# Performance work log

Measured on AMD Instinct MI355X. Metric: run time of the kernel, lower is better.

Reference implementation:

```python
import jax, jax.numpy as jnp
import numpy as np

B = 512      # batch per stream
L = 600      # audio length (22 chunks of 75, step 25)
DIM = 256    # model dim
H = 8        # num heads (each head is full-width, per original code)
CH = [1, DIM // 4, DIM // 2, DIM]
KS = [26, 26, 25]
EPS = 1e-5
N_CHUNKS, CHUNK, STEP = 22, 75, 25


def setup_inputs() -> dict:
    key = jax.random.key(0)
    ks = iter(jax.random.split(key, 40))
    def rn(shape, scale=0.05):
        return jax.random.normal(next(ks), shape, jnp.float32) * scale
    inp = {}
    inp["audio_vec1"] = jax.random.normal(next(ks), (B, 1, L), jnp.float32)
    inp["audio_vec2"] = jax.random.normal(next(ks), (B, 1, L), jnp.float32)
    for i in range(3):
        inp[f"conv_w{i+1}"] = rn((CH[i + 1], CH[i], KS[i]))  # OIH, torch Conv1d layout
        inp[f"conv_b{i+1}"] = rn((CH[i + 1],))
        inp[f"bn_g{i+1}"] = jnp.ones((CH[i + 1],), jnp.float32)
        inp[f"bn_b{i+1}"] = jnp.zeros((CH[i + 1],), jnp.float32)
        inp[f"bn_m{i+1}"] = rn((CH[i + 1],))
        inp[f"bn_v{i+1}"] = jnp.ones((CH[i + 1],), jnp.float32)
    # per-head Q/K/V projections (stored [H, in, out]; torch Linear is x @ W.T + b)
    inp["Wq"] = rn((H, DIM, DIM)); inp["bq"] = rn((H, DIM))
    inp["Wk"] = rn((H, DIM, DIM)); inp["bk"] = rn((H, DIM))
    inp["Wv"] = rn((H, DIM, DIM)); inp["bv"] = rn((H, DIM))
    inp["fca_w"] = rn((H * DIM, DIM)); inp["fca_b"] = rn((DIM,))
    inp["fc_w"] = rn((DIM, DIM)); inp["fc_b"] = rn((DIM,))
    return inp


def _chunks(x):
    # x: [B, 1, L] -> [B*22, 1, 75] (batched chunks, chunk-major within each example)
    idx = jnp.arange(N_CHUNKS)[:, None] * STEP + jnp.arange(CHUNK)[None, :]  # [22, 75]
    c = x[:, :, idx]                      # [B, 1, 22, 75]
    return c.transpose(0, 2, 1, 3).reshape(-1, 1, CHUNK)


def _block(x, w, b, g, bt, m, v):
    # Conv1d (valid) + BatchNorm (eval) + Swish; dropout is identity in eval.
    y = jax.lax.conv_general_dilated(
        x, w, window_strides=(1,), padding="VALID",
        dimension_numbers=("NCH", "OIH", "NCH")) + b[None, :, None]
    scale = g * jax.lax.rsqrt(v + EPS)
    y = (y - m[None, :, None]) * scale[None, :, None] + bt[None, :, None]
    return y * jax.nn.sigmoid(y)


def _forward(audio_vec1, audio_vec2,
             conv_w1, conv_b1, bn_g1, bn_b1, bn_m1, bn_v1,
             conv_w2, conv_b2, bn_g2, bn_b2, bn_m2, bn_v2,
             conv_w3, conv_b3, bn_g3, bn_b3, bn_m3, bn_v3,
             Wq, bq, Wk, bk, Wv, bv, fca_w, fca_b, fc_w, fc_b):
    # Batch both streams and all 22 chunks through one conv stack.
    X = jnp.concatenate([_chunks(audio_vec1), _chunks(audio_vec2)], axis=0)  # [2*B*22,1,75]
    X = _block(X, conv_w1, conv_b1, bn_g1, bn_b1, bn_m1, bn_v1)  # [., 64, 50]
    X = _block(X, conv_w2, conv_b2, bn_g2, bn_b2, bn_m2, bn_v2)  # [., 128, 25]
    X = _block(X, conv_w3, conv_b3, bn_g3, bn_b3, bn_m3, bn_v3)  # [., 256, 1]
    feat = X[:, :, 0].reshape(-1, N_CHUNKS, DIM)  # [2B, 22, 256]

    # Multi-head attention: 8 independent full-width heads, no 1/sqrt(d) scaling.
    Q = jnp.einsum("bse,heo->bhso", feat, Wq) + bq[None, :, None, :]
    K = jnp.einsum("bse,heo->bhso", feat, Wk) + bk[None, :, None, :]
    V = jnp.einsum("bse,heo->bhso", feat, Wv) + bv[None, :, None, :]
    A = jax.nn.softmax(jnp.einsum("bhso,bhto->bhst", Q, K), axis=-1)
    O = jnp.einsum("bhst,bhto->bhso", A, V)          # [2B, H, 22, 256]
    O = O.transpose(0, 2, 1, 3).reshape(O.shape[0], N_CHUNKS, H * DIM)
    out = O @ fca_w + fca_b                            # [2B, 22, 256]

    pooled = out.mean(axis=1)                          # [2B, 256]
    y = pooled @ fc_w + fc_b                           # [2B, 256]
    nb = audio_vec1.shape[0]
    return y[:nb], y[nb:]


def reference(audio_vec1, audio_vec2,
              conv_w1, conv_b1, bn_g1, bn_b1, bn_m1, bn_v1,
              conv_w2, conv_b2, bn_g2, bn_b2, bn_m2, bn_v2,
              conv_w3, conv_b3, bn_g3, bn_b3, bn_m3, bn_v3,
              Wq, bq, Wk, bk, Wv, bv, fca_w, fca_b, fc_w, fc_b):
    return _forward(audio_vec1, audio_vec2,
                    conv_w1, conv_b1, bn_g1, bn_b1, bn_m1, bn_v1,
                    conv_w2, conv_b2, bn_g2, bn_b2, bn_m2, bn_v2,
                    conv_w3, conv_b3, bn_g3, bn_b3, bn_m3, bn_v3,
                    Wq, bq, Wk, bk, Wv, bv, fca_w, fca_b, fc_w, fc_b)
```

## Files before the change

kernel.cpp:

```cpp
#include <hip/hip_runtime.h>
#include <hip/hip_bf16.h>
#include <math.h>

#define NSEQ 22528
#define HALFSEQ 11264

typedef __attribute__((ext_vector_type(8))) short short8;
typedef __attribute__((ext_vector_type(4))) float f32x4;
typedef __attribute__((ext_vector_type(4))) ushort ushort4v;

__device__ __forceinline__ ushort f2bf(float x) {
    __hip_bfloat16 h = __float2bfloat16(x);
    return *reinterpret_cast<ushort*>(&h);
}
__device__ __forceinline__ float bf2f(ushort u) {
    unsigned v = ((unsigned)u) << 16;
    return *reinterpret_cast<float*>(&v);
}

__global__ void k_transpose(const float* __restrict__ in, float* __restrict__ out,
                            int Bn, int R, int C) {
    int idx = blockIdx.x * 256 + threadIdx.x;
    int total = Bn * R * C;
    if (idx >= total) return;
    int b = idx / (R * C);
    int rem = idx - b * R * C;
    int c = rem / R;
    int r = rem - c * R;
    out[idx] = in[(b * R + r) * C + c];
}

__global__ void k_prep_w2(const float* __restrict__ w2, ushort* __restrict__ w2f) {
    int idx = blockIdx.x * 256 + threadIdx.x;
    if (idx >= 212992) return;
    int j = idx & 7;
    int lane = (idx >> 3) & 63;
    int mt = (idx >> 9) & 7;
    int kt = idx >> 12;
    int oc = mt * 16 + (lane & 15);
    int k = kt * 32 + ((lane >> 4) << 3) + j;
    int t = k >> 6;
    int ic = k & 63;
    w2f[idx] = f2bf(w2[(oc * 64 + ic) * 26 + t]);
}
__global__ void k_prep_w3(const float* __restrict__ w3, ushort* __restrict__ w3f) {
    int idx = blockIdx.x * 256 + threadIdx.x;
    if (idx >= 819200) return;
    int j = idx & 7;
    int lane = (idx >> 3) & 63;
    int mt = (idx >> 9) & 15;
    int kt = idx >> 13;
    int oc = mt * 16 + (lane & 15);
    int k = kt * 32 + ((lane >> 4) << 3) + j;
    int ic = k & 127;
    int pos = k >> 7;
    w3f[idx] = f2bf(w3[oc * 3200 + ic * 25 + pos]);
}

__global__ __launch_bounds__(256) void k_prep_attn_m(
    const float* __restrict__ Wq, const float* __restrict__ WkT,
    float* __restrict__ M)
{
    const int h = blockIdx.x >> 4;
    const int e0 = (blockIdx.x & 15) * 16;
    const int tid = threadIdx.x;
    __shared__ float sq[16][256];
    for (int idx = tid; idx < 4096; idx += 256) {
        int r = idx >> 8;
        int c = idx & 255;
        sq[r][c] = Wq[(size_t)(h * 256 + e0 + r) * 256 + c];
    }
    __syncthreads();
    float acc[16];
    #pragma unroll
    for (int r = 0; r < 16; ++r) acc[r] = 0.f;
    const float* wkt = WkT + (size_t)h * 65536 + tid;
    for (int o = 0; o < 256; ++o) {
        float wk = wkt[o * 256];
        #pragma unroll
        for (int r = 0; r < 16; ++r) acc[r] += sq[r][o] * wk;
    }
    #pragma unroll
    for (int r = 0; r < 16; ++r)
        M[(size_t)(h * 256 + e0 + r) * 256 + tid] = acc[r];
}

__global__ void k_prep_mfrag(const float* __restrict__ M, ushort* __restrict__ Mfrag) {
    int idx = blockIdx.x * 256 + threadIdx.x;
    int j = idx & 7;
    int lane = (idx >> 3) & 63;
    int mt = (idx >> 9) & 15;
    int kt = (idx >> 13) & 7;
    int h = idx >> 16;
    int e = kt * 32 + ((lane >> 4) << 3) + j;
    int o = mt * 16 + (lane & 15);
    Mfrag[idx] = f2bf(M[(size_t)(h * 256 + e) * 256 + o]);
}

__global__ __launch_bounds__(256) void k_prep_kb(
    const float* __restrict__ Wk, const float* __restrict__ bq,
    float* __restrict__ kb)
{
    const int h = blockIdx.x;
    const int tid = threadIdx.x;
    __shared__ float sbq[256];
    sbq[tid] = bq[h * 256 + tid];
    __syncthreads();
    const float* wk = Wk + (size_t)(h * 256 + tid) * 256;
    float a = 0.f;
    for (int o = 0; o < 256; ++o) a += wk[o] * sbq[o];
    kb[h * 256 + tid] = a;
}

__global__ __launch_bounds__(256) void k_prep_F(
    const float* __restrict__ Wv, const float* __restrict__ fca_w,
    float* __restrict__ F)
{
    const int h = blockIdx.x >> 4;
    const int e0 = (blockIdx.x & 15) * 16;
    const int tid = threadIdx.x;
    __shared__ float sq[16][256];
    for (int idx = tid; idx < 4096; idx += 256) {
        int r = idx >> 8;
        int c = idx & 255;
        sq[r][c] = Wv[(size_t)h * 65536 + (e0 + r) * 256 + c];
    }
    __syncthreads();
    float acc[16];
    #pragma unroll
    for (int r = 0; r < 16; ++r) acc[r] = 0.f;
    for (int o = 0; o < 256; ++o) {
        float w = fca_w[(size_t)(h * 256 + o) * 256 + tid];
        #pragma unroll
        for (int r = 0; r < 16; ++r) acc[r] += sq[r][o] * w;
    }
    #pragma unroll
    for (int r = 0; r < 16; ++r)
        F[(size_t)(h * 256 + e0 + r) * 256 + tid] = acc[r];
}

__global__ __launch_bounds__(256) void k_prep_bvc(
    const float* __restrict__ bv, const float* __restrict__ fca_w,
    const float* __restrict__ fca_b, float* __restrict__ bvc)
{
    const int tid = threadIdx.x;
    __shared__ float sbv[2048];
    for (int i = tid; i < 2048; i += 256) sbv[i] = bv[i];
    __syncthreads();
    float acc = fca_b[tid];
    for (int k = 0; k < 2048; ++k) acc += sbv[k] * fca_w[(size_t)k * 256 + tid];
    bvc[tid] = acc;
}

__global__ __launch_bounds__(256, 4) void k_conv(
    const float* __restrict__ av1, const float* __restrict__ av2,
    const float* __restrict__ w1,
    const float* __restrict__ b1c, const float* __restrict__ g1,
    const float* __restrict__ be1, const float* __restrict__ m1, const float* __restrict__ v1,
    const ushort* __restrict__ w2f,
    const float* __restrict__ b2c, const float* __restrict__ g2,
    const float* __restrict__ be2, const float* __restrict__ m2, const float* __restrict__ v2,
    ushort* __restrict__ a2f, int seqoff)
{
    __shared__ ushort s_a1[4 * 3200];
    __shared__ ushort s_w1f[2048];
    __shared__ ushort s_xb[4][80];
    __shared__ float s_sc1[64], s_sh1[64], s_sc2[128], s_sh2[128];

    const int tid = threadIdx.x;
    const int lane = tid & 63;
    const int wv = tid >> 6;
    const int l15 = lane & 15;
    const int grp = lane >> 4;
    const int lseq0 = blockIdx.x * 4;
    const int gseq0 = seqoff + lseq0;

    for (int s = 0; s < 4; ++s) {
        int seq = gseq0 + s;
        const float* src;
        if (seq < HALFSEQ) { int b = seq / 22; int n = seq - b * 22; src = av1 + b * 600 + n * 25; }
        else { int q = seq - HALFSEQ; int b = q / 22; int n = q - b * 22; src = av2 + b * 600 + n * 25; }
        if (tid < 80) s_xb[s][tid] = f2bf((tid < 75) ? src[tid] : 0.f);
    }
    for (int idx = tid; idx < 2048; idx += 256) {
        int j = idx & 7;
        int ln = (idx >> 3) & 63;
        int mt = idx >> 9;
        int oc = mt * 16 + (ln & 15);
        int k = ((ln >> 4) << 3) + j;
        s_w1f[idx] = (k < 26) ? f2bf(w1[oc * 26 + k]) : (ushort)0;
    }
    if (tid < 64) { float A = g1[tid] * rsqrtf(v1[tid] + 1e-5f); s_sc1[tid] = A; s_sh1[tid] = (b1c[tid] - m1[tid]) * A + be1[tid]; }
    if (tid < 128) { float A = g2[tid] * rsqrtf(v2[tid] + 1e-5f); s_sc2[tid] = A; s_sh2[tid] = (b2c[tid] - m2[tid]) * A + be2[tid]; }
    __syncthreads();

    {
        short8 a1f[4];
        #pragma unroll
        for (int mt = 0; mt < 4; ++mt)
            a1f[mt] = *(const short8*)(s_w1f + mt * 512 + lane * 8);

        for (int nt = wv; nt < 13; nt += 4) {
            int n = nt * 16 + l15;
            int s = (n >= 50) + (n >= 100) + (n >= 150);
            int p = n - s * 50;
            if (p > 49) p = 49;
            short8 bf;
            #pragma unroll
            for (int j = 0; j < 8; ++j) {
                int t = grp * 8 + j;
                bf[j] = (t < 26) ? (short)s_xb[s][p + t] : (short)0;
            }
            f32x4 acc1[4];
            #pragma unroll
            for (int mt = 0; mt < 4; ++mt) {
                acc1[mt] = (f32x4){0.f, 0.f, 0.f, 0.f};
                acc1[mt] = __builtin_amdgcn_mfma_f32_16x16x32_bf16(a1f[mt], bf, acc1[mt], 0, 0, 0);
            }
            if (n < 200) {
                #pragma unroll
                for (int mt = 0; mt < 4; ++mt) {
                    #pragma unroll
                    for (int r = 0; r < 4; ++r) {
                        int oc = mt * 16 + grp * 4 + r;
                        float y = acc1[mt][r] * s_sc1[oc] + s_sh1[oc];
                        y = y / (1.f + __expf(-y));
                        int boff = s * 6400 + p * 128 + ((oc * 2) ^ ((p & 7) << 4));
                        *(ushort*)((char*)s_a1 + boff) = f2bf(y);
                    }
                }
            }
        }
    }
    __syncthreads();

    {
        const int mset = wv >> 1;
        const int nset = wv & 1;
        const int NT = nset ? 3 : 4;

        int nbase[4], nrow[4];
        #pragma unroll
        for (int ni = 0; ni < 4; ++ni) {
            int n = (nset * 4 + ni) * 16 + l15;
            int s = n / 25; if (s > 3) s = 3;
            int p = n - s * 25; if (p > 24) p = 24;
            nbase[ni] = s * 6400;
            nrow[ni] = p;
        }

        f32x4 acc[4][4];
        #pragma unroll
        for (int mi = 0; mi < 4; ++mi)
            #pragma unroll
            for (int ni = 0; ni < 4; ++ni)
                acc[mi][ni] = (f32x4){0.f, 0.f, 0.f, 0.f};

        const ushort* wfp = w2f + (size_t)(mset * 4) * 512 + lane * 8;
        short8 afn[4];
        #pragma unroll
        for (int mi = 0; mi < 4; ++mi) afn[mi] = *(const short8*)(wfp + mi * 512);

        for (int kt = 0; kt < 52; ++kt) {
            const int t = kt >> 1;
            const int ic0b = ((kt & 1) * 32 + grp * 8) * 2;
            short8 af[4];
            #pragma unroll
            for (int mi = 0; mi < 4; ++mi) af[mi] = afn[mi];
            if (kt < 51) {
                #pragma unroll
                for (int mi = 0; mi < 4; ++mi)
                    afn[mi] = *(const short8*)(wfp + (kt + 1) * 4096 + mi * 512);
            }
            #pragma unroll
            for (int ni = 0; ni < 4; ++ni) {
                if (ni >= NT) break;
                int row = nrow[ni] + t;
                int boff = nbase[ni] + row * 128 + (ic0b ^ ((row & 7) << 4));
                short8 bf = *(const short8*)((const char*)s_a1 + boff);
                #pragma unroll
                for (int mi = 0; mi < 4; ++mi)
                    acc[mi][ni] = __builtin_amdgcn_mfma_f32_16x16x32_bf16(af[mi], bf, acc[mi][ni], 0, 0, 0);
            }
        }

        #pragma unroll
        for (int mi = 0; mi < 4; ++mi) {
            const int ocb = mset * 64 + mi * 16 + grp * 4;
            const int grp_dst = (ocb & 31) >> 3;
            const int jb = ocb & 7;
            const int kthi = ocb >> 5;
            #pragma unroll
            for (int ni = 0; ni < 4; ++ni) {
                if (ni >= NT) break;
                int n = (nset * 4 + ni) * 16 + l15;
                if (n < 100) {
                    int s = n / 25;
                    int p = n - s * 25;
                    int seq = lseq0 + s;
                    int kt3 = p * 4 + kthi;
                    ushort4v u;
                    #pragma unroll
                    for (int r = 0; r < 4; ++r) {
                        float y = acc[mi][ni][r] * s_sc2[ocb + r] + s_sh2[ocb + r];
                        y = y / (1.f + __expf(-y));
                        u[r] = f2bf(y);
                    }
                    *(ushort4v*)(a2f + (((size_t)(seq >> 4) * 100 + kt3) << 9)
                                 + ((seq & 15) + 16 * grp_dst) * 8 + jb) = u;
                }
            }
        }
    }
}

__global__ __launch_bounds__(256) void k_conv3(
    const ushort* __restrict__ a2f, const ushort* __restrict__ w3f,
    const float* __restrict__ b3c, const float* __restrict__ g3,
    const float* __restrict__ be3, const float* __restrict__ m3, const float* __restrict__ v3,
    float* __restrict__ feat, int seqoff)
{
    const int tid = threadIdx.x;
    const int lane = tid & 63;
    const int wv = tid >> 6;
    const int l15 = lane & 15;
    const int grp = lane >> 4;
    const int lseq0 = blockIdx.x * 32;

    f32x4 acc3[4][2];
    #pragma unroll
    for (int mi = 0; mi < 4; ++mi)
        #pragma unroll
        for (int nt = 0; nt < 2; ++nt)
            acc3[mi][nt] = (f32x4){0.f, 0.f, 0.f, 0.f};

    const ushort* bp = a2f + ((size_t)(lseq0 >> 4) * 100) * 512 + lane * 8;
    const ushort* ap = w3f + (size_t)(wv * 4) * 512 + lane * 8;

    for (int kt = 0; kt < 100; ++kt) {
        short8 bf0 = *(const short8*)(bp + (size_t)kt * 512);
        short8 bf1 = *(const short8*)(bp + (size_t)(100 + kt) * 512);
        #pragma unroll
        for (int mi = 0; mi < 4; ++mi) {
            short8 af = *(const short8*)(ap + (size_t)kt * 8192 + mi * 512);
            acc3[mi][0] = __builtin_amdgcn_mfma_f32_16x16x32_bf16(af, bf0, acc3[mi][0], 0, 0, 0);
            acc3[mi][1] = __builtin_amdgcn_mfma_f32_16x16x32_bf16(af, bf1, acc3[mi][1], 0, 0, 0);
        }
    }

    #pragma unroll
    for (int nt = 0; nt < 2; ++nt) {
        int gseq = seqoff + lseq0 + nt * 16 + l15;
        #pragma unroll
        for (int mi = 0; mi < 4; ++mi) {
            int oc = wv * 64 + mi * 16 + grp * 4;
            float4 o4;
            #pragma unroll
            for (int r = 0; r < 4; ++r) {
                float A = g3[oc + r] * rsqrtf(v3[oc + r] + 1e-5f);
                float y = acc3[mi][nt][r] * A + (b3c[oc + r] - m3[oc + r]) * A + be3[oc + r];
                ((float*)&o4)[r] = y / (1.f + __expf(-y));
            }
            *(float4*)(feat + (size_t)gseq * 256 + oc) = o4;
        }
    }
}

__global__ __launch_bounds__(256, 2) void k_attn_f(
    const float* __restrict__ feat, const ushort* __restrict__ Mfrag,
    const float* __restrict__ kb, float* __restrict__ fbar_all)
{
    const int g = blockIdx.x;
    const int tid = threadIdx.x;
    const int lane = tid & 63;
    const int wv = tid >> 6;
    const int l15 = lane & 15;
    const int grp = lane >> 4;

    __shared__ __align__(16) float sfL[22 * 260];
    __shared__ __align__(16) ushort sfb[32 * 256];
    __shared__ __align__(16) ushort sG[32 * 256];
    __shared__ float sS[22 * 24];
    __shared__ float sbet[8][24];
    __shared__ float sab[24];

    const float* fsrc = feat + (size_t)g * 5632;
    for (int idx = tid; idx < 8192; idx += 256) {
        int s = idx >> 8;
        int e = idx & 255;
        float f = 0.f;
        if (s < 22) { f = fsrc[s * 256 + e]; sfL[s * 260 + e] = f; }
        int byte = s * 512 + ((e * 2) ^ ((s & 7) << 4));
        *(ushort*)((char*)sfb + byte) = f2bf(f);
    }
    __syncthreads();

    if (tid < 176) {
        int t = tid >> 3;
        int h = tid & 7;
        const float* kr = kb + h * 256;
        const float* fr = sfL + t * 260;
        float a = 0.f;
        for (int e = 0; e < 256; ++e) a += fr[e] * kr[e];
        sbet[h][t] = a;
    }
    __syncthreads();

    for (int h = 0; h < 8; ++h) {
        {
            f32x4 accg[2][4];
            #pragma unroll
            for (int mt = 0; mt < 2; ++mt)
                #pragma unroll
                for (int fi = 0; fi < 4; ++fi)
                    accg[mt][fi] = (f32x4){0.f, 0.f, 0.f, 0.f};

            const ushort* mfb = Mfrag + (size_t)h * 65536;
            for (int kt = 0; kt < 8; ++kt) {
                int e0b = (kt * 32 + grp * 8) * 2;
                int rA0 = l15, rA1 = 16 + l15;
                short8 af0 = *(const short8*)((const char*)sfb + rA0 * 512 + (e0b ^ ((rA0 & 7) << 4)));
                short8 af1 = *(const short8*)((const char*)sfb + rA1 * 512 + (e0b ^ ((rA1 & 7) << 4)));
                #pragma unroll
                for (int fi = 0; fi < 4; ++fi) {
                    int ft = wv * 4 + fi;
                    short8 bfm = *(const short8*)(mfb + (size_t)((kt * 16 + ft) << 9) + lane * 8);
                    accg[0][fi] = __builtin_amdgcn_mfma_f32_16x16x32_bf16(af0, bfm, accg[0][fi], 0, 0, 0);
                    accg[1][fi] = __builtin_amdgcn_mfma_f32_16x16x32_bf16(af1, bfm, accg[1][fi], 0, 0, 0);
                }
            }
            #pragma unroll
            for (int mt = 0; mt < 2; ++mt) {
                #pragma unroll
                for (int fi = 0; fi < 4; ++fi) {
                    int f = (wv * 4 + fi) * 16 + l15;
                    #pragma unroll
                    for (int r = 0; r < 4; ++r) {
                        int s = mt * 16 + grp * 4 + r;
                        if (s < 22) {
                            int byte = s * 512 + ((f * 2) ^ ((s & 7) << 4));
                            *(ushort*)((char*)sG + byte) = f2bf(accg[mt][fi][r]);
                        }
                    }
                }
            }
        }
        __syncthreads();

        {
            int mt2 = wv >> 1;
            int nt2 = wv & 1;
            f32x4 sacc = (f32x4){0.f, 0.f, 0.f, 0.f};
            int sA = mt2 * 16 + l15;
            int tB = nt2 * 16 + l15;
            for (int kt = 0; kt < 8; ++kt) {
                int f0b = (kt * 32 + grp * 8) * 2;
                short8 ga = *(const short8*)((const char*)sG + sA * 512 + (f0b ^ ((sA & 7) << 4)));
                short8 fb = *(const short8*)((const char*)sfb + tB * 512 + (f0b ^ ((tB & 7) << 4)));
                sacc = __builtin_amdgcn_mfma_f32_16x16x32_bf16(ga, fb, sacc, 0, 0, 0);
            }
            #pragma unroll
            for (int r = 0; r < 4; ++r) {
                int s = mt2 * 16 + grp * 4 + r;
                int t = nt2 * 16 + l15;
                if (s < 22 && t < 22) sS[s * 24 + t] = sacc[r] + sbet[h][t];
            }
        }
        __syncthreads();

        if (tid < 22) {
            int s = tid;
            float mx = -1e30f;
            #pragma unroll
            for (int t = 0; t < 22; ++t) mx = fmaxf(mx, sS[s * 24 + t]);
            float ex[22];
            float sum = 0.f;
            #pragma unroll
            for (int t = 0; t < 22; ++t) { float e2 = __expf(sS[s * 24 + t] - mx); ex[t] = e2; sum += e2; }
            float inv = 1.f / sum;
            #pragma unroll
            for (int t = 0; t < 22; ++t) sS[s * 24 + t] = ex[t] * inv;
        }
        __syncthreads();
        if (tid < 22) {
            int t = tid;
            float a = 0.f;
            #pragma unroll
            for (int s = 0; s < 22; ++s) a += sS[s * 24 + t];
            sab[t] = a * (1.f / 22.f);
        }
        __syncthreads();

        {
            float a = 0.f;
            #pragma unroll
            for (int t = 0; t < 22; ++t) a += sab[t] * sfL[t * 260 + tid];
            fbar_all[((size_t)g * 8 + h) * 256 + tid] = a;
        }
    }
}

__global__ __launch_bounds__(256) void k_pool(
    const float* __restrict__ fbar_all, const float* __restrict__ F,
    const float* __restrict__ bvc,
    const float* __restrict__ fc_w, const float* __restrict__ fc_b,
    float* __restrict__ out)
{
    const int g0 = blockIdx.x * 4;
    const int tid = threadIdx.x;
    __shared__ __align__(16) float sfb[32 * 256];
    __shared__ __align__(16) float sp[4 * 256];
    for (int idx = tid; idx < 8192; idx += 256)
        sfb[idx] = fbar_all[(size_t)g0 * 8 * 256 + idx];
    __syncthreads();

    float p[4];
    float bb = bvc[tid];
    #pragma unroll
    for (int j = 0; j < 4; ++j) p[j] = bb;
    for (int k = 0; k < 2048; ++k) {
        float f = F[(size_t)k * 256 + tid];
        #pragma unroll
        for (int j = 0; j < 4; ++j) p[j] += sfb[j * 2048 + k] * f;
    }
    #pragma unroll
    for (int j = 0; j < 4; ++j) sp[j * 256 + tid] = p[j];
    __syncthreads();

    float y[4];
    float fb = fc_b[tid];
    #pragma unroll
    for (int j = 0; j < 4; ++j) y[j] = fb;
    for (int e = 0; e < 256; ++e) {
        float w = fc_w[(size_t)e * 256 + tid];
        #pragma unroll
        for (int j = 0; j < 4; ++j) y[j] += sp[j * 256 + e] * w;
    }
    #pragma unroll
    for (int j = 0; j < 4; ++j)
        out[(size_t)(g0 + j) * 256 + tid] = y[j];
}

extern "C" void kernel_launch(void* const* d_in, const int* in_sizes, int n_in,
                              void* d_out, int out_size, void* d_ws, size_t ws_size,
                              hipStream_t stream) {
    (void)in_sizes; (void)n_in; (void)out_size;

    const float* av1   = (const float*)d_in[0];
    const float* av2   = (const float*)d_in[1];
    const float* w1    = (const float*)d_in[2];
    const float* b1c   = (const float*)d_in[3];
    const float* g1    = (const float*)d_in[4];
    const float* be1   = (const float*)d_in[5];
    const float* m1    = (const float*)d_in[6];
    const float* v1    = (const float*)d_in[7];
    const float* w2    = (const float*)d_in[8];
    const float* b2c   = (const float*)d_in[9];
    const float* g2    = (const float*)d_in[10];
    const float* be2   = (const float*)d_in[11];
    const float* m2    = (const float*)d_in[12];
    const float* v2    = (const float*)d_in[13];
    const float* w3    = (const float*)d_in[14];
    const float* b3c   = (const float*)d_in[15];
    const float* g3    = (const float*)d_in[16];
    const float* be3   = (const float*)d_in[17];
    const float* m3    = (const float*)d_in[18];
    const float* v3    = (const float*)d_in[19];
    const float* Wq    = (const float*)d_in[20];
    const float* bq    = (const float*)d_in[21];
    const float* Wk    = (const float*)d_in[22];
    const float* bk    = (const float*)d_in[23];
    const float* Wv    = (const float*)d_in[24];
    const float* bv    = (const float*)d_in[25];
    const float* fca_w = (const float*)d_in[26];
    const float* fca_b = (const float*)d_in[27];
    const float* fc_w  = (const float*)d_in[28];
    const float* fc_b  = (const float*)d_in[29];
    (void)bk;

    float* ws = (float*)d_ws;
    float* feat = ws;
    float* Mm   = feat + 5767168;
    float* WkT  = Mm + 524288;
    float* kb   = WkT + 524288;
    float* bvc  = kb + 2048;
    float* F    = bvc + 256;
    float* fbar = F + 524288;
    ushort* w2f = (ushort*)(fbar + 2097152);
    ushort* w3f = w2f + 212992;
    ushort* mfr = w3f + 819200;
    ushort* region = mfr + 524288;

    size_t base_bytes = (size_t)((char*)region - (char*)d_ws);
    size_t budget = (ws_size > base_bytes + 4096) ? (ws_size - base_bytes - 4096) : 0;
    int ncA = 16;
    const int cand[5] = {1, 2, 4, 8, 16};
    for (int i = 0; i < 5; ++i) { if ((size_t)144179200 / cand[i] <= budget) { ncA = cand[i]; break; } }
    const int seqsA = NSEQ / ncA;

    k_prep_w2<<<832, 256, 0, stream>>>(w2, w2f);
    k_prep_w3<<<3200, 256, 0, stream>>>(w3, w3f);
    k_transpose<<<2048, 256, 0, stream>>>(Wk, WkT, 8, 256, 256);
    k_prep_attn_m<<<128, 256, 0, stream>>>(Wq, WkT, Mm);
    k_prep_mfrag<<<2048, 256, 0, stream>>>(Mm, mfr);
    k_prep_kb<<<8, 256, 0, stream>>>(Wk, bq, kb);
    k_prep_F<<<128, 256, 0, stream>>>(Wv, fca_w, F);
    k_prep_bvc<<<1, 256, 0, stream>>>(bv, fca_w, fca_b, bvc);

    ushort* a2f = region;
    for (int c = 0; c < ncA; ++c) {
        int seqoff = c * seqsA;
        k_conv<<<seqsA / 4, 256, 0, stream>>>(av1, av2,
            w1, b1c, g1, be1, m1, v1,
            w2f, b2c, g2, be2, m2, v2,
            a2f, seqoff);
        k_conv3<<<seqsA / 32, 256, 0, stream>>>(a2f, w3f,
            b3c, g3, be3, m3, v3, feat, seqoff);
    }

    k_attn_f<<<1024, 256, 0, stream>>>(feat, mfr, kb, fbar);
    k_pool<<<256, 256, 0, stream>>>(fbar, F, bvc, fc_w, fc_b, (float*)d_out);
}
```

Before: 666.3 us.

## Merge prep kernels, widen conv2 block to 8 sequences, enlarge conv3 tile

```diff
diff --git a/kernel.cpp b/kernel.cpp
--- a/kernel.cpp
+++ b/kernel.cpp
@@ -18,43 +18,88 @@
     return *reinterpret_cast<float*>(&v);
 }
 
-__global__ void k_transpose(const float* __restrict__ in, float* __restrict__ out,
-                            int Bn, int R, int C) {
-    int idx = blockIdx.x * 256 + threadIdx.x;
-    int total = Bn * R * C;
-    if (idx >= total) return;
-    int b = idx / (R * C);
-    int rem = idx - b * R * C;
-    int c = rem / R;
-    int r = rem - c * R;
-    out[idx] = in[(b * R + r) * C + c];
-}
-
-__global__ void k_prep_w2(const float* __restrict__ w2, ushort* __restrict__ w2f) {
-    int idx = blockIdx.x * 256 + threadIdx.x;
-    if (idx >= 212992) return;
-    int j = idx & 7;
-    int lane = (idx >> 3) & 63;
-    int mt = (idx >> 9) & 7;
-    int kt = idx >> 12;
-    int oc = mt * 16 + (lane & 15);
-    int k = kt * 32 + ((lane >> 4) << 3) + j;
-    int t = k >> 6;
-    int ic = k & 63;
-    w2f[idx] = f2bf(w2[(oc * 64 + ic) * 26 + t]);
-}
-__global__ void k_prep_w3(const float* __restrict__ w3, ushort* __restrict__ w3f) {
-    int idx = blockIdx.x * 256 + threadIdx.x;
-    if (idx >= 819200) return;
-    int j = idx & 7;
-    int lane = (idx >> 3) & 63;
-    int mt = (idx >> 9) & 15;
-    int kt = idx >> 13;
-    int oc = mt * 16 + (lane & 15);
-    int k = kt * 32 + ((lane >> 4) << 3) + j;
-    int ic = k & 127;
-    int pos = k >> 7;
-    w3f[idx] = f2bf(w3[oc * 3200 + ic * 25 + pos]);
+__global__ __launch_bounds__(256) void k_prep_misc(
+    const float* __restrict__ w2, ushort* __restrict__ w2f,
+    const float* __restrict__ w3, ushort* __restrict__ w3f,
+    const float* __restrict__ Wk, float* __restrict__ WkT,
+    const float* __restrict__ bq, float* __restrict__ kb,
+    const float* __restrict__ bv, const float* __restrict__ fca_w,
+    const float* __restrict__ fca_b, float* __restrict__ bvc,
+    const float* __restrict__ Wv, float* __restrict__ F)
+{
+    __shared__ float smem[16 * 256];
+    const int bid = blockIdx.x;
+    const int tid = threadIdx.x;
+
+    if (bid < 832) {
+        int idx = bid * 256 + tid;
+        if (idx < 212992) {
+            int j = idx & 7;
+            int lane = (idx >> 3) & 63;
+            int mt = (idx >> 9) & 7;
+            int kt = idx >> 12;
+            int oc = mt * 16 + (lane & 15);
+            int k = kt * 32 + ((lane >> 4) << 3) + j;
+            int t = k >> 6;
+            int ic = k & 63;
+            w2f[idx] = f2bf(w2[(oc * 64 + ic) * 26 + t]);
+        }
+    } else if (bid < 4032) {
+        int idx = (bid - 832) * 256 + tid;
+        if (idx < 819200) {
+            int j = idx & 7;
+            int lane = (idx >> 3) & 63;
+            int mt = (idx >> 9) & 15;
+            int kt = idx >> 13;
+            int oc = mt * 16 + (lane & 15);
+            int k = kt * 32 + ((lane >> 4) << 3) + j;
+            int ic = k & 127;
+            int pos = k >> 7;
+            w3f[idx] = f2bf(w3[oc * 3200 + ic * 25 + pos]);
+        }
+    } else if (bid < 6080) {
+        int idx = (bid - 4032) * 256 + tid;
+        int b = idx >> 16;
+        int rem = idx & 65535;
+        int c = rem >> 8;
+        int r = rem & 255;
+        WkT[idx] = Wk[(size_t)(b * 256 + r) * 256 + c];
+    } else if (bid < 6088) {
+        int h = bid - 6080;
+        smem[tid] = bq[h * 256 + tid];
+        __syncthreads();
+        const float* wk = Wk + (size_t)(h * 256 + tid) * 256;
+        float a = 0.f;
+        for (int o = 0; o < 256; ++o) a += wk[o] * smem[o];
+        kb[h * 256 + tid] = a;
+    } else if (bid < 6089) {
+        for (int i = tid; i < 2048; i += 256) smem[i] = bv[i];
+        __syncthreads();
+        float acc = fca_b[tid];
+        for (int k = 0; k < 2048; ++k) acc += smem[k] * fca_w[(size_t)k * 256 + tid];
+        bvc[tid] = acc;
+    } else {
+        int lb = bid - 6089;
+        int h = lb >> 4;
+        int e0 = (lb & 15) * 16;
+        for (int idx = tid; idx < 4096; idx += 256) {
+            int r = idx >> 8;
+            int c = idx & 255;
+            smem[r * 256 + c] = Wv[(size_t)h * 65536 + (e0 + r) * 256 + c];
+        }
+        __syncthreads();
+        float acc[16];
+        #pragma unroll
+        for (int r = 0; r < 16; ++r) acc[r] = 0.f;
+        for (int o = 0; o < 256; ++o) {
+            float w = fca_w[(size_t)(h * 256 + o) * 256 + tid];
+            #pragma unroll
+            for (int r = 0; r < 16; ++r) acc[r] += smem[r * 256 + o] * w;
+        }
+        #pragma unroll
+        for (int r = 0; r < 16; ++r)
+            F[(size_t)(h * 256 + e0 + r) * 256 + tid] = acc[r];
+    }
 }
 
 __global__ __launch_bounds__(256) void k_prep_attn_m(
@@ -97,62 +142,7 @@
     Mfrag[idx] = f2bf(M[(size_t)(h * 256 + e) * 256 + o]);
 }
 
-__global__ __launch_bounds__(256) void k_prep_kb(
-    const float* __restrict__ Wk, const float* __restrict__ bq,
-    float* __restrict__ kb)
-{
-    const int h = blockIdx.x;
-    const int tid = threadIdx.x;
-    __shared__ float sbq[256];
-    sbq[tid] = bq[h * 256 + tid];
-    __syncthreads();
-    const float* wk = Wk + (size_t)(h * 256 + tid) * 256;
-    float a = 0.f;
-    for (int o = 0; o < 256; ++o) a += wk[o] * sbq[o];
-    kb[h * 256 + tid] = a;
-}
-
-__global__ __launch_bounds__(256) void k_prep_F(
-    const float* __restrict__ Wv, const float* __restrict__ fca_w,
-    float* __restrict__ F)
-{
-    const int h = blockIdx.x >> 4;
-    const int e0 = (blockIdx.x & 15) * 16;
-    const int tid = threadIdx.x;
-    __shared__ float sq[16][256];
-    for (int idx = tid; idx < 4096; idx += 256) {
-        int r = idx >> 8;
-        int c = idx & 255;
-        sq[r][c] = Wv[(size_t)h * 65536 + (e0 + r) * 256 + c];
-    }
-    __syncthreads();
-    float acc[16];
-    #pragma unroll
-    for (int r = 0; r < 16; ++r) acc[r] = 0.f;
-    for (int o = 0; o < 256; ++o) {
-        float w = fca_w[(size_t)(h * 256 + o) * 256 + tid];
-        #pragma unroll
-        for (int r = 0; r < 16; ++r) acc[r] += sq[r][o] * w;
-    }
-    #pragma unroll
-    for (int r = 0; r < 16; ++r)
-        F[(size_t)(h * 256 + e0 + r) * 256 + tid] = acc[r];
-}
-
-__global__ __launch_bounds__(256) void k_prep_bvc(
-    const float* __restrict__ bv, const float* __restrict__ fca_w,
-    const float* __restrict__ fca_b, float* __restrict__ bvc)
-{
-    const int tid = threadIdx.x;
-    __shared__ float sbv[2048];
-    for (int i = tid; i < 2048; i += 256) sbv[i] = bv[i];
-    __syncthreads();
-    float acc = fca_b[tid];
-    for (int k = 0; k < 2048; ++k) acc += sbv[k] * fca_w[(size_t)k * 256 + tid];
-    bvc[tid] = acc;
-}
-
-__global__ __launch_bounds__(256, 4) void k_conv(
+__global__ __launch_bounds__(512, 4) void k_conv(
     const float* __restrict__ av1, const float* __restrict__ av2,
     const float* __restrict__ w1,
     const float* __restrict__ b1c, const float* __restrict__ g1,
@@ -162,27 +152,29 @@
     const float* __restrict__ be2, const float* __restrict__ m2, const float* __restrict__ v2,
     ushort* __restrict__ a2f, int seqoff)
 {
-    __shared__ ushort s_a1[4 * 3200];
+    __shared__ ushort s_a1[8 * 3200];
     __shared__ ushort s_w1f[2048];
-    __shared__ ushort s_xb[4][80];
+    __shared__ ushort s_xb[8][80];
     __shared__ float s_sc1[64], s_sh1[64], s_sc2[128], s_sh2[128];
 
     const int tid = threadIdx.x;
     const int lane = tid & 63;
-    const int wv = tid >> 6;
+    const int w = tid >> 6;
     const int l15 = lane & 15;
     const int grp = lane >> 4;
-    const int lseq0 = blockIdx.x * 4;
+    const int lseq0 = blockIdx.x * 8;
     const int gseq0 = seqoff + lseq0;
 
-    for (int s = 0; s < 4; ++s) {
+    for (int idx = tid; idx < 640; idx += 512) {
+        int s = idx / 80;
+        int i = idx - s * 80;
         int seq = gseq0 + s;
         const float* src;
         if (seq < HALFSEQ) { int b = seq / 22; int n = seq - b * 22; src = av1 + b * 600 + n * 25; }
         else { int q = seq - HALFSEQ; int b = q / 22; int n = q - b * 22; src = av2 + b * 600 + n * 25; }
-        if (tid < 80) s_xb[s][tid] = f2bf((tid < 75) ? src[tid] : 0.f);
-    }
-    for (int idx = tid; idx < 2048; idx += 256) {
+        s_xb[s][i] = f2bf((i < 75) ? src[i] : 0.f);
+    }
+    for (int idx = tid; idx < 2048; idx += 512) {
         int j = idx & 7;
         int ln = (idx >> 3) & 63;
         int mt = idx >> 9;
@@ -191,7 +183,10 @@
         s_w1f[idx] = (k < 26) ? f2bf(w1[oc * 26 + k]) : (ushort)0;
     }
     if (tid < 64) { float A = g1[tid] * rsqrtf(v1[tid] + 1e-5f); s_sc1[tid] = A; s_sh1[tid] = (b1c[tid] - m1[tid]) * A + be1[tid]; }
-    if (tid < 128) { float A = g2[tid] * rsqrtf(v2[tid] + 1e-5f); s_sc2[tid] = A; s_sh2[tid] = (b2c[tid] - m2[tid]) * A + be2[tid]; }
+    if (tid >= 128 && tid < 256) {
+        int o = tid - 128;
+        float A = g2[o] * rsqrtf(v2[o] + 1e-5f); s_sc2[o] = A; s_sh2[o] = (b2c[o] - m2[o]) * A + be2[o];
+    }
     __syncthreads();
 
     {
@@ -200,101 +195,103 @@
         for (int mt = 0; mt < 4; ++mt)
             a1f[mt] = *(const short8*)(s_w1f + mt * 512 + lane * 8);
 
-        for (int nt = wv; nt < 13; nt += 4) {
+        for (int nt = w; nt < 25; nt += 8) {
             int n = nt * 16 + l15;
-            int s = (n >= 50) + (n >= 100) + (n >= 150);
+            int s = n / 50;
             int p = n - s * 50;
-            if (p > 49) p = 49;
             short8 bf;
             #pragma unroll
             for (int j = 0; j < 8; ++j) {
                 int t = grp * 8 + j;
                 bf[j] = (t < 26) ? (short)s_xb[s][p + t] : (short)0;
             }
-            f32x4 acc1[4];
             #pragma unroll
             for (int mt = 0; mt < 4; ++mt) {
-                acc1[mt] = (f32x4){0.f, 0.f, 0.f, 0.f};
-                acc1[mt] = __builtin_amdgcn_mfma_f32_16x16x32_bf16(a1f[mt], bf, acc1[mt], 0, 0, 0);
-            }
-            if (n < 200) {
+                f32x4 acc1 = (f32x4){0.f, 0.f, 0.f, 0.f};
+                acc1 = __builtin_amdgcn_mfma_f32_16x16x32_bf16(a1f[mt], bf, acc1, 0, 0, 0);
+                int oc0 = mt * 16 + grp * 4;
+                int icb = oc0 >> 3;
+                int boff = s * 6400 + icb * 800 + p * 16 + (oc0 & 7) * 2;
+                ushort4v u;
                 #pragma unroll
-                for (int mt = 0; mt < 4; ++mt) {
-                    #pragma unroll
-                    for (int r = 0; r < 4; ++r) {
-                        int oc = mt * 16 + grp * 4 + r;
-                        float y = acc1[mt][r] * s_sc1[oc] + s_sh1[oc];
-                        y = y / (1.f + __expf(-y));
-                        int boff = s * 6400 + p * 128 + ((oc * 2) ^ ((p & 7) << 4));
-                        *(ushort*)((char*)s_a1 + boff) = f2bf(y);
-                    }
+                for (int r = 0; r < 4; ++r) {
+                    float y = acc1[r] * s_sc1[oc0 + r] + s_sh1[oc0 + r];
+                    y = y / (1.f + __expf(-y));
+                    u[r] = f2bf(y);
                 }
+                *(ushort4v*)((char*)s_a1 + boff) = u;
             }
         }
     }
     __syncthreads();
 
     {
-        const int mset = wv >> 1;
-        const int nset = wv & 1;
-        const int NT = nset ? 3 : 4;
-
-        int nbase[4], nrow[4];
-        #pragma unroll
-        for (int ni = 0; ni < 4; ++ni) {
-            int n = (nset * 4 + ni) * 16 + l15;
-            int s = n / 25; if (s > 3) s = 3;
+        const int mset = w & 3;
+        const int nset = w >> 2;
+        const int NT = nset ? 6 : 7;
+
+        int vaddr[7];
+        #pragma unroll
+        for (int ni = 0; ni < 7; ++ni) {
+            int nt = nset * 7 + ni;
+            int n = nt * 16 + l15;
+            int s = n / 25; if (s > 7) s = 7;
             int p = n - s * 25; if (p > 24) p = 24;
-            nbase[ni] = s * 6400;
-            nrow[ni] = p;
-        }
-
-        f32x4 acc[4][4];
-        #pragma unroll
-        for (int mi = 0; mi < 4; ++mi)
-            #pragma unroll
-            for (int ni = 0; ni < 4; ++ni)
+            vaddr[ni] = s * 6400 + grp * 800 + p * 16;
+        }
+
+        f32x4 acc[2][7];
+        #pragma unroll
+        for (int mi = 0; mi < 2; ++mi)
+            #pragma unroll
+            for (int ni = 0; ni < 7; ++ni)
                 acc[mi][ni] = (f32x4){0.f, 0.f, 0.f, 0.f};
 
-        const ushort* wfp = w2f + (size_t)(mset * 4) * 512 + lane * 8;
-        short8 afn[4];
-        #pragma unroll
-        for (int mi = 0; mi < 4; ++mi) afn[mi] = *(const short8*)(wfp + mi * 512);
-
-        for (int kt = 0; kt < 52; ++kt) {
-            const int t = kt >> 1;
-            const int ic0b = ((kt & 1) * 32 + grp * 8) * 2;
-            short8 af[4];
-            #pragma unroll
-            for (int mi = 0; mi < 4; ++mi) af[mi] = afn[mi];
-            if (kt < 51) {
-                #pragma unroll
-                for (int mi = 0; mi < 4; ++mi)
-                    afn[mi] = *(const short8*)(wfp + (kt + 1) * 4096 + mi * 512);
-            }
-            #pragma unroll
-            for (int ni = 0; ni < 4; ++ni) {
+        const ushort* wpt = w2f + (size_t)(mset * 2) * 512 + lane * 8;
+        short8 afA0 = *(const short8*)(wpt);
+        short8 afA1 = *(const short8*)(wpt + 512);
+        short8 afB0 = *(const short8*)(wpt + 4096);
+        short8 afB1 = *(const short8*)(wpt + 4096 + 512);
+
+        for (int t = 0; t < 26; ++t) {
+            #pragma unroll
+            for (int ni = 0; ni < 7; ++ni) {
                 if (ni >= NT) break;
-                int row = nrow[ni] + t;
-                int boff = nbase[ni] + row * 128 + (ic0b ^ ((row & 7) << 4));
-                short8 bf = *(const short8*)((const char*)s_a1 + boff);
-                #pragma unroll
-                for (int mi = 0; mi < 4; ++mi)
-                    acc[mi][ni] = __builtin_amdgcn_mfma_f32_16x16x32_bf16(af[mi], bf, acc[mi][ni], 0, 0, 0);
-            }
-        }
-
-        #pragma unroll
-        for (int mi = 0; mi < 4; ++mi) {
-            const int ocb = mset * 64 + mi * 16 + grp * 4;
-            const int grp_dst = (ocb & 31) >> 3;
+                short8 bf = *(const short8*)((const char*)s_a1 + vaddr[ni]);
+                acc[0][ni] = __builtin_amdgcn_mfma_f32_16x16x32_bf16(afA0, bf, acc[0][ni], 0, 0, 0);
+                acc[1][ni] = __builtin_amdgcn_mfma_f32_16x16x32_bf16(afA1, bf, acc[1][ni], 0, 0, 0);
+            }
+            if (t < 25) {
+                afA0 = *(const short8*)(wpt + 8192);
+                afA1 = *(const short8*)(wpt + 8192 + 512);
+            }
+            #pragma unroll
+            for (int ni = 0; ni < 7; ++ni) {
+                if (ni >= NT) break;
+                short8 bf = *(const short8*)((const char*)s_a1 + vaddr[ni] + 3200);
+                acc[0][ni] = __builtin_amdgcn_mfma_f32_16x16x32_bf16(afB0, bf, acc[0][ni], 0, 0, 0);
+                acc[1][ni] = __builtin_amdgcn_mfma_f32_16x16x32_bf16(afB1, bf, acc[1][ni], 0, 0, 0);
+            }
+            if (t < 25) {
+                afB0 = *(const short8*)(wpt + 12288);
+                afB1 = *(const short8*)(wpt + 12288 + 512);
+                wpt += 8192;
+            }
+            #pragma unroll
+            for (int ni = 0; ni < 7; ++ni) vaddr[ni] += 16;
+        }
+
+        #pragma unroll
+        for (int mi = 0; mi < 2; ++mi) {
+            const int ocb = mset * 32 + mi * 16 + grp * 4;
+            const int grp_dst = (ocb >> 3) & 3;
             const int jb = ocb & 7;
             const int kthi = ocb >> 5;
             #pragma unroll
-            for (int ni = 0; ni < 4; ++ni) {
+            for (int ni = 0; ni < 7; ++ni) {
                 if (ni >= NT) break;
-                int n = (nset * 4 + ni) * 16 + l15;
-                if (n < 100) {
+                int n = (nset * 7 + ni) * 16 + l15;
+                if (n < 200) {
                     int s = n / 25;
                     int p = n - s * 25;
                     int seq = lseq0 + s;
@@ -325,31 +322,34 @@
     const int wv = tid >> 6;
     const int l15 = lane & 15;
     const int grp = lane >> 4;
-    const int lseq0 = blockIdx.x * 32;
-
-    f32x4 acc3[4][2];
+    const int lseq0 = blockIdx.x * 64;
+
+    f32x4 acc3[4][4];
     #pragma unroll
     for (int mi = 0; mi < 4; ++mi)
         #pragma unroll
-        for (int nt = 0; nt < 2; ++nt)
+        for (int nt = 0; nt < 4; ++nt)
             acc3[mi][nt] = (f32x4){0.f, 0.f, 0.f, 0.f};
 
     const ushort* bp = a2f + ((size_t)(lseq0 >> 4) * 100) * 512 + lane * 8;
     const ushort* ap = w3f + (size_t)(wv * 4) * 512 + lane * 8;
 
     for (int kt = 0; kt < 100; ++kt) {
-        short8 bf0 = *(const short8*)(bp + (size_t)kt * 512);
-        short8 bf1 = *(const short8*)(bp + (size_t)(100 + kt) * 512);
+        short8 bf[4];
+        #pragma unroll
+        for (int nt = 0; nt < 4; ++nt)
+            bf[nt] = *(const short8*)(bp + (size_t)(nt * 100 + kt) * 512);
         #pragma unroll
         for (int mi = 0; mi < 4; ++mi) {
             short8 af = *(const short8*)(ap + (size_t)kt * 8192 + mi * 512);
-            acc3[mi][0] = __builtin_amdgcn_mfma_f32_16x16x32_bf16(af, bf0, acc3[mi][0], 0, 0, 0);
-            acc3[mi][1] = __builtin_amdgcn_mfma_f32_16x16x32_bf16(af, bf1, acc3[mi][1], 0, 0, 0);
-        }
-    }
-
-    #pragma unroll
-    for (int nt = 0; nt < 2; ++nt) {
+            #pragma unroll
+            for (int nt = 0; nt < 4; ++nt)
+                acc3[mi][nt] = __builtin_amdgcn_mfma_f32_16x16x32_bf16(af, bf[nt], acc3[mi][nt], 0, 0, 0);
+        }
+    }
+
+    #pragma unroll
+    for (int nt = 0; nt < 4; ++nt) {
         int gseq = seqoff + lseq0 + nt * 16 + l15;
         #pragma unroll
         for (int mi = 0; mi < 4; ++mi) {
@@ -598,23 +598,19 @@
     for (int i = 0; i < 5; ++i) { if ((size_t)144179200 / cand[i] <= budget) { ncA = cand[i]; break; } }
     const int seqsA = NSEQ / ncA;
 
-    k_prep_w2<<<832, 256, 0, stream>>>(w2, w2f);
-    k_prep_w3<<<3200, 256, 0, stream>>>(w3, w3f);
-    k_transpose<<<2048, 256, 0, stream>>>(Wk, WkT, 8, 256, 256);
+    k_prep_misc<<<6217, 256, 0, stream>>>(w2, w2f, w3, w3f, Wk, WkT,
+                                          bq, kb, bv, fca_w, fca_b, bvc, Wv, F);
     k_prep_attn_m<<<128, 256, 0, stream>>>(Wq, WkT, Mm);
     k_prep_mfrag<<<2048, 256, 0, stream>>>(Mm, mfr);
-    k_prep_kb<<<8, 256, 0, stream>>>(Wk, bq, kb);
-    k_prep_F<<<128, 256, 0, stream>>>(Wv, fca_w, F);
-    k_prep_bvc<<<1, 256, 0, stream>>>(bv, fca_w, fca_b, bvc);
 
     ushort* a2f = region;
     for (int c = 0; c < ncA; ++c) {
         int seqoff = c * seqsA;
-        k_conv<<<seqsA / 4, 256, 0, stream>>>(av1, av2,
+        k_conv<<<seqsA / 8, 512, 0, stream>>>(av1, av2,
             w1, b1c, g1, be1, m1, v1,
             w2f, b2c, g2, be2, m2, v2,
             a2f, seqoff);
-        k_conv3<<<seqsA / 32, 256, 0, stream>>>(a2f, w3f,
+        k_conv3<<<seqsA / 64, 256, 0, stream>>>(a2f, w3f,
             b3c, g3, be3, m3, v3, feat, seqoff);
     }
 
```

After: 601.4 us. 1.11x faster.
